# Kernel optimization log

Measured on AMD Instinct MI355X. Metric: run time of the kernel, lower is better.

The kernel has to match this reference:

```python
import jax, jax.numpy as jnp
import numpy as np

VOCAB, EMBED = 50000, 256
MODULES, HEADS, HID = 2, 4, 64
B, S = 8, 2048
LABELS = 16


def setup_inputs() -> dict:
    key = jax.random.key(0)
    ks = jax.random.split(key, 12)
    seqs = jax.random.randint(ks[0], (B, S), 0, VOCAB)
    emb = jax.random.normal(ks[1], (VOCAB, EMBED), jnp.float32) * 0.02
    Wq = jax.random.normal(ks[2], (MODULES, HEADS, HID, EMBED), jnp.float32) * (1.0 / np.sqrt(EMBED))
    bq = jax.random.normal(ks[3], (MODULES, HEADS, HID), jnp.float32) * 0.01
    Wk = jax.random.normal(ks[4], (MODULES, HEADS, HID, EMBED), jnp.float32) * (1.0 / np.sqrt(EMBED))
    bk = jax.random.normal(ks[5], (MODULES, HEADS, HID), jnp.float32) * 0.01
    Wv = jax.random.normal(ks[6], (MODULES, HEADS, HID, EMBED), jnp.float32) * (1.0 / np.sqrt(EMBED))
    bv = jax.random.normal(ks[7], (MODULES, HEADS, HID), jnp.float32) * 0.01
    Wz = jax.random.normal(ks[8], (MODULES, EMBED, HEADS * HID), jnp.float32) * (1.0 / np.sqrt(HEADS * HID))
    bz = jax.random.normal(ks[9], (MODULES, EMBED), jnp.float32) * 0.01
    Wo = jax.random.normal(ks[10], (LABELS, S * EMBED), jnp.float32) * (1.0 / np.sqrt(S * EMBED))
    bo = jax.random.normal(ks[11], (LABELS,), jnp.float32) * 0.01
    return {"seqs": seqs, "emb": emb, "Wq": Wq, "bq": bq, "Wk": Wk, "bk": bk,
            "Wv": Wv, "bv": bv, "Wz": Wz, "bz": bz, "Wo": Wo, "bo": bo}


def _forward(seqs, emb, Wq, bq, Wk, bk, Wv, bv, Wz, bz, Wo, bo):
    x = emb[seqs]  # [B, S, E]
    scale = jnp.float32(EMBED) ** 0.5
    for m in range(MODULES):
        # per-head projections with relu (dropout=0 / eval mode)
        Q = jax.nn.relu(jnp.einsum('bse,hde->bhsd', x, Wq[m]) + bq[m][None, :, None, :])
        K = jax.nn.relu(jnp.einsum('bse,hde->bhsd', x, Wk[m]) + bk[m][None, :, None, :])
        V = jax.nn.relu(jnp.einsum('bse,hde->bhsd', x, Wv[m]) + bv[m][None, :, None, :])
        QK = jnp.einsum('bhsd,bhtd->bhst', Q, K) / scale  # [B,H,S,S]
        # double softmax: first over the query axis (torch dim=1 of [B,S,S]),
        # then over the key axis (torch dim=2)
        A = jax.nn.softmax(QK, axis=2)
        A = jax.nn.softmax(A, axis=3)
        Z = jnp.einsum('bhst,bhtd->bhsd', A, V)  # [B,H,S,HID]
        Zall = jnp.transpose(Z, (0, 2, 1, 3)).reshape(x.shape[0], S, HEADS * HID)
        ZF = jnp.einsum('bsk,ek->bse', Zall, Wz[m]) + bz[m]
        x = ZF + x  # residual (layer_norm=False)
    Xf = x.reshape(x.shape[0], S * EMBED)
    y = jax.nn.sigmoid(Xf @ Wo.T + bo)
    return y


def reference(seqs, emb, Wq, bq, Wk, bk, Wv, bv, Wz, bz, Wo, bo):
    return _forward(seqs, emb, Wq, bq, Wk, bk, Wv, bv, Wz, bz, Wo, bo)
```

## Files before the change

### kernel.cpp

```cpp
#include <hip/hip_runtime.h>
#include <math.h>

#define Bb 8
#define Ss 2048
#define Ee 256
#define Hh 4
#define Dd 64

typedef unsigned short u16;
typedef unsigned int u32;
typedef __attribute__((ext_vector_type(8))) short bf16x8;
typedef __attribute__((ext_vector_type(4))) float f32x4;
typedef __attribute__((ext_vector_type(16))) float f32x16;

__device__ __forceinline__ u16 f2bf(float f) {
  union { float f; u32 u; } c; c.f = f;
  return (u16)((c.u + 0x7FFFu + ((c.u >> 16) & 1u)) >> 16);
}
__device__ __forceinline__ float bf2f(u16 u) {
  union { u32 u; float f; } c; c.u = ((u32)u) << 16;
  return c.f;
}
__device__ __forceinline__ float bf2fs(short s) { return bf2f((u16)s); }
__device__ __forceinline__ u32 cvtpk(float a, float b) {
  u32 r;
  asm("v_cvt_pk_bf16_f32 %0, %1, %2" : "=v"(r) : "v"(a), "v"(b));
  return r;
}
__device__ __forceinline__ float ex2(float x) { return __builtin_amdgcn_exp2f(x); }

__global__ __launch_bounds__(256) void k_w2b(const float* __restrict__ src,
                                             u16* __restrict__ dst) {
  int idx = (blockIdx.x * 256 + threadIdx.x) * 4;
  float4 v = *reinterpret_cast<const float4*>(src + idx);
  ushort4 o;
  o.x = f2bf(v.x); o.y = f2bf(v.y); o.z = f2bf(v.z); o.w = f2bf(v.w);
  *reinterpret_cast<ushort4*>(dst + idx) = o;
}

__global__ __launch_bounds__(256) void k_gather(const int* __restrict__ seqs,
                                                const float* __restrict__ emb,
                                                float* __restrict__ x,
                                                u16* __restrict__ xb) {
  int idx = blockIdx.x * 256 + threadIdx.x;
  int row = idx >> 6, c4 = idx & 63;
  int tok = seqs[row];
  float4 v = reinterpret_cast<const float4*>(emb)[(size_t)tok * 64 + c4];
  reinterpret_cast<float4*>(x)[(size_t)row * 64 + c4] = v;
  ushort4 o;
  o.x = f2bf(v.x); o.y = f2bf(v.y); o.z = f2bf(v.z); o.w = f2bf(v.w);
  reinterpret_cast<ushort4*>(xb)[(size_t)row * 64 + c4] = o;
}

__global__ __launch_bounds__(256) void k_qkvm(const u16* __restrict__ xb,
    const u16* __restrict__ Wqb, const u16* __restrict__ Wkb, const u16* __restrict__ Wvb,
    const float* __restrict__ bq, const float* __restrict__ bk, const float* __restrict__ bv,
    u16* __restrict__ Qf, u16* __restrict__ Kf, u16* __restrict__ Vf, int mod) {
  __shared__ short Xs[128][72];
  __shared__ short Ws[128][72];
  int tid = threadIdx.x;
  int bn = blockIdx.x;
  int arr = bn >> 1, coff = (bn & 1) << 7;
  const u16* W = (arr == 0 ? Wqb : arr == 1 ? Wkb : Wvb) + (size_t)mod * 256 * 256;
  const float* bias = (arr == 0 ? bq : arr == 1 ? bk : bv) + mod * 256;
  u16* Out = (arr == 0 ? Qf : arr == 1 ? Kf : Vf);
  float oscale = (arr == 0) ? 0.0625f * 1.44269504f : 1.0f;
  int s0 = blockIdx.y * 128;
  int lr = tid >> 1, lc = (tid & 1) << 5;
  int w = tid >> 6, lane = tid & 63, ml = lane & 15, q = lane >> 4;
  int sh = (w >> 1) << 6, th = (w & 1) << 6;
  f32x4 acc[4][4] = {};
  for (int k0 = 0; k0 < 256; k0 += 64) {
#pragma unroll
    for (int hh = 0; hh < 4; hh++) {
      *reinterpret_cast<bf16x8*>(&Xs[lr][lc + hh * 8]) =
          *reinterpret_cast<const bf16x8*>(xb + (size_t)(s0 + lr) * Ee + k0 + lc + hh * 8);
      *reinterpret_cast<bf16x8*>(&Ws[lr][lc + hh * 8]) =
          *reinterpret_cast<const bf16x8*>(W + (size_t)(coff + lr) * Ee + k0 + lc + hh * 8);
    }
    __syncthreads();
#pragma unroll
    for (int ks = 0; ks < 2; ks++) {
      bf16x8 af[4], bfr[4];
#pragma unroll
      for (int mt = 0; mt < 4; mt++)
        af[mt] = *reinterpret_cast<const bf16x8*>(&Xs[sh + mt * 16 + ml][ks * 32 + q * 8]);
#pragma unroll
      for (int nt = 0; nt < 4; nt++)
        bfr[nt] = *reinterpret_cast<const bf16x8*>(&Ws[th + nt * 16 + ml][ks * 32 + q * 8]);
#pragma unroll
      for (int mt = 0; mt < 4; mt++)
#pragma unroll
        for (int nt = 0; nt < 4; nt++)
          acc[mt][nt] = __builtin_amdgcn_mfma_f32_16x16x32_bf16(af[mt], bfr[nt], acc[mt][nt], 0, 0, 0);
    }
    __syncthreads();
  }
#pragma unroll
  for (int mt = 0; mt < 4; mt++)
#pragma unroll
    for (int nt = 0; nt < 4; nt++)
#pragma unroll
      for (int r = 0; r < 4; r++) {
        int gm = s0 + sh + mt * 16 + q * 4 + r;
        int cc = coff + th + nt * 16 + ml;
        float v = acc[mt][nt][r] + bias[cc];
        v = (v > 0.f ? v : 0.f) * oscale;
        Out[(size_t)gm * Ee + cc] = f2bf(v);
      }
}

__global__ __launch_bounds__(256) void k_vt(const u16* __restrict__ Vf,
                                            u16* __restrict__ Vt) {
  __shared__ u16 T[64][72];
  int tid = threadIdx.x;
  int t0 = blockIdx.x * 64;
  int z = blockIdx.y;
  int b = z >> 2, h = z & 3;
  int lr = tid >> 2, lc = (tid & 3) << 4;
#pragma unroll
  for (int hh = 0; hh < 2; hh++) {
    bf16x8 v = *reinterpret_cast<const bf16x8*>(
        Vf + (size_t)(b * Ss + t0 + lr) * Ee + h * Dd + lc + hh * 8);
#pragma unroll
    for (int j = 0; j < 8; j++) T[lr][lc + hh * 8 + j] = (u16)v[j];
  }
  __syncthreads();
#pragma unroll
  for (int j = 0; j < 16; j++) {
    Vt[((size_t)z * Dd + lr) * Ss + t0 + lc + j] = T[lc + j][lr];
  }
}

__global__ __launch_bounds__(256) void k_vsum(const u16* __restrict__ Vt,
                                              float* __restrict__ SV,
                                              float* __restrict__ csums) {
  int gi = (blockIdx.y * gridDim.x + blockIdx.x) * 256 + threadIdx.x;
  if (gi < 32 * Ss) csums[gi] = 0.f;
  int z = blockIdx.y;
  int d = blockIdx.x * 4 + (threadIdx.x >> 6);
  int lane = threadIdx.x & 63;
  const u16* row = Vt + ((size_t)z * Dd + d) * Ss;
  float s = 0.f;
#pragma unroll
  for (int it = 0; it < 4; it++) {
    bf16x8 v = *reinterpret_cast<const bf16x8*>(row + it * 512 + lane * 8);
#pragma unroll
    for (int j = 0; j < 8; j++) s += bf2fs(v[j]);
  }
#pragma unroll
  for (int off = 32; off; off >>= 1) s += __shfl_xor(s, off);
  if (lane == 0) SV[(size_t)z * Dd + d] = s;
}

__global__ __launch_bounds__(256, 4) void k_csum(const u16* __restrict__ Qf,
    const u16* __restrict__ Kf, float* __restrict__ csums) {
  __shared__ float csm[2][128];
  int tid = threadIdx.x;
  int lin = (blockIdx.z * 2 + blockIdx.y) * 16 + blockIdx.x;
  int wgid = (lin & 7) * 128 + (lin >> 3);
  int ttile = wgid & 15, shalf = (wgid >> 4) & 1, z = wgid >> 5;
  int b = z >> 2, h = z & 3;
  const u16* Qb = Qf + (size_t)b * Ss * Ee + h * Dd;
  const u16* Kb = Kf + (size_t)b * Ss * Ee + h * Dd;
  int w = tid >> 6, lane = tid & 63, l31 = lane & 31, hi = lane >> 5;
  int sh = (w >> 1) << 6, th = (w & 1) << 6;
  const u16* kr = Kb + (size_t)(ttile * 128 + th + l31) * Ee + hi * 8;
  bf16x8 kb[2][4];
#pragma unroll
  for (int tt = 0; tt < 2; tt++)
#pragma unroll
    for (int kk = 0; kk < 4; kk++)
      kb[tt][kk] = *reinterpret_cast<const bf16x8*>(kr + (size_t)tt * 32 * Ee + kk * 16);
  float cs0 = 0.f, cs1 = 0.f;
  int sBeg = shalf * 1024, sEnd = sBeg + 1024;
  for (int s0 = sBeg; s0 < sEnd; s0 += 128) {
#pragma unroll
    for (int qs = 0; qs < 2; qs++) {
      const u16* Qr = Qb + (size_t)(s0 + sh + qs * 32 + l31) * Ee + hi * 8;
      f32x16 a0 = {}, a1 = {};
      __builtin_amdgcn_s_setprio(1);
#pragma unroll
      for (int kk = 0; kk < 4; kk++) {
        bf16x8 qv = *reinterpret_cast<const bf16x8*>(Qr + kk * 16);
        a0 = __builtin_amdgcn_mfma_f32_32x32x16_bf16(qv, kb[0][kk], a0, 0, 0, 0);
        a1 = __builtin_amdgcn_mfma_f32_32x32x16_bf16(qv, kb[1][kk], a1, 0, 0, 0);
      }
      __builtin_amdgcn_s_setprio(0);
#pragma unroll
      for (int j = 0; j < 16; j++) { cs0 += ex2(a0[j]); cs1 += ex2(a1[j]); }
    }
  }
  cs0 += __shfl_xor(cs0, 32);
  cs1 += __shfl_xor(cs1, 32);
  if (lane < 32) {
    csm[w >> 1][th + l31] = cs0;
    csm[w >> 1][th + 32 + l31] = cs1;
  }
  __syncthreads();
  if (tid < 128)
    atomicAdd(&csums[(size_t)z * Ss + ttile * 128 + tid], csm[0][tid] + csm[1][tid]);
}

__global__ void k_llog(float* __restrict__ llic) {
  int i = blockIdx.x * 256 + threadIdx.x;
  llic[i] = -__log2f(llic[i]);
}

__global__ __launch_bounds__(256, 4) void k_att(const u16* __restrict__ Qf,
    const u16* __restrict__ Kf, const u16* __restrict__ Vt,
    const float* __restrict__ llic, const float* __restrict__ SV,
    u16* __restrict__ Zb) {
  __shared__ short Vs[2][64 * 72];
  __shared__ short A2s[64 * 72];
  __shared__ float rs_s[2][64];
  int tid = threadIdx.x;
  int lin = blockIdx.y * 32 + blockIdx.x;
  int wgid = (lin & 7) * 128 + (lin >> 3);
  int z = wgid >> 5, sblk = wgid & 31;
  int b = z >> 2, h = z & 3;
  const u16* Qb = Qf + (size_t)b * Ss * Ee + h * Dd;
  const u16* Kb = Kf + (size_t)b * Ss * Ee + h * Dd;
  const u16* VtZ = Vt + (size_t)z * Dd * Ss;
  const float* lz = llic + (size_t)z * Ss;
  int s0 = sblk * 64;
  int w = tid >> 6, lane = tid & 63;
  int l31 = lane & 31, hi = lane >> 5;
  int tw = w >> 1, sw = w & 1;
  const u16* qrow = Qb + (size_t)(s0 + sw * 32 + l31) * Ee + hi * 8;
  bf16x8 qb0 = *reinterpret_cast<const bf16x8*>(qrow);
  bf16x8 qb1 = *reinterpret_cast<const bf16x8*>(qrow + 16);
  bf16x8 qb2 = *reinterpret_cast<const bf16x8*>(qrow + 32);
  bf16x8 qb3 = *reinterpret_cast<const bf16x8*>(qrow + 48);
  const u16* krow = Kb + (size_t)(tw * 32 + l31) * Ee + hi * 8;
  bf16x8 kf0 = *reinterpret_cast<const bf16x8*>(krow);
  bf16x8 kf1 = *reinterpret_cast<const bf16x8*>(krow + 16);
  bf16x8 kf2 = *reinterpret_cast<const bf16x8*>(krow + 32);
  bf16x8 kf3 = *reinterpret_cast<const bf16x8*>(krow + 48);
  int sd = tid >> 2, sg = (tid & 3) << 4;
  {
    const u16* vsrc = VtZ + (size_t)sd * Ss + sg;
    *reinterpret_cast<bf16x8*>(&Vs[0][sd * 72 + sg]) = *reinterpret_cast<const bf16x8*>(vsrc);
    *reinterpret_cast<bf16x8*>(&Vs[0][sd * 72 + sg + 8]) = *reinterpret_cast<const bf16x8*>(vsrc + 8);
  }
  f32x16 acc2 = {};
  float rsv = 0.f;
  int pb = 0;
  short* arow = &A2s[(sw * 32 + l31) * 72 + tw * 32];
  const short* a2row = &A2s[(tw * 32 + l31) * 72 + hi * 8];
  for (int t0 = 0; t0 < Ss; t0 += 64) {
    f32x16 at = {};
    __builtin_amdgcn_s_setprio(1);
    at = __builtin_amdgcn_mfma_f32_32x32x16_bf16(kf0, qb0, at, 0, 0, 0);
    at = __builtin_amdgcn_mfma_f32_32x32x16_bf16(kf1, qb1, at, 0, 0, 0);
    at = __builtin_amdgcn_mfma_f32_32x32x16_bf16(kf2, qb2, at, 0, 0, 0);
    at = __builtin_amdgcn_mfma_f32_32x32x16_bf16(kf3, qb3, at, 0, 0, 0);
    __builtin_amdgcn_s_setprio(0);
    int tn = (t0 + 64 < Ss) ? t0 + 64 : 0;
    {
      const u16* krn = krow + (size_t)tn * Ee;
      kf0 = *reinterpret_cast<const bf16x8*>(krn);
      kf1 = *reinterpret_cast<const bf16x8*>(krn + 16);
      kf2 = *reinterpret_cast<const bf16x8*>(krn + 32);
      kf3 = *reinterpret_cast<const bf16x8*>(krn + 48);
    }
#pragma unroll
    for (int g = 0; g < 4; g++) {
      const float4 lc = *reinterpret_cast<const float4*>(lz + t0 + tw * 32 + g * 8 + hi * 4);
      float e0 = ex2(at[g * 4 + 0] + lc.x);
      float e1 = ex2(at[g * 4 + 1] + lc.y);
      float e2 = ex2(at[g * 4 + 2] + lc.z);
      float e3 = ex2(at[g * 4 + 3] + lc.w);
      float p0 = e0 * (1.f + e0 * (0.5f + e0 * (0.166666667f + e0 * 0.0416666667f)));
      float p1 = e1 * (1.f + e1 * (0.5f + e1 * (0.166666667f + e1 * 0.0416666667f)));
      float p2 = e2 * (1.f + e2 * (0.5f + e2 * (0.166666667f + e2 * 0.0416666667f)));
      float p3 = e3 * (1.f + e3 * (0.5f + e3 * (0.166666667f + e3 * 0.0416666667f)));
      rsv += (p0 + p1) + (p2 + p3);
      uint2 pk;
      pk.x = cvtpk(p0, p1);
      pk.y = cvtpk(p2, p3);
      *reinterpret_cast<uint2*>(arow + g * 8 + hi * 4) = pk;
    }
    __syncthreads();
    {
      const u16* vsrc = VtZ + (size_t)sd * Ss + tn + sg;
      bf16x8 v0 = *reinterpret_cast<const bf16x8*>(vsrc);
      bf16x8 v1 = *reinterpret_cast<const bf16x8*>(vsrc + 8);
      short* vdst = &Vs[pb ^ 1][sd * 72 + sg];
      *reinterpret_cast<bf16x8*>(vdst) = v0;
      *reinterpret_cast<bf16x8*>(vdst + 8) = v1;
    }
    {
      const short* vrow = &Vs[pb][(sw * 32 + l31) * 72 + hi * 8];
      __builtin_amdgcn_s_setprio(1);
#pragma unroll
      for (int kk = 0; kk < 4; kk++) {
        bf16x8 af2 = *reinterpret_cast<const bf16x8*>(a2row + kk * 16);
        bf16x8 bvv = *reinterpret_cast<const bf16x8*>(vrow + kk * 16);
        acc2 = __builtin_amdgcn_mfma_f32_32x32x16_bf16(af2, bvv, acc2, 0, 0, 0);
      }
      __builtin_amdgcn_s_setprio(0);
    }
    __syncthreads();
    pb ^= 1;
  }
  rsv += __shfl_xor(rsv, 32);
  if (lane < 32) rs_s[tw][sw * 32 + l31] = rsv;
  __syncthreads();
  float svd = SV[(size_t)z * Dd + sw * 32 + l31];
#pragma unroll
  for (int g = 0; g < 4; g++)
#pragma unroll
    for (int rr = 0; rr < 4; rr++) {
      int row = tw * 32 + g * 8 + hi * 4 + rr;
      float inv = 1.f / (2048.f + rs_s[0][row] + rs_s[1][row]);
      float o = (svd + acc2[g * 4 + rr]) * inv;
      Zb[(size_t)(b * Ss + s0 + row) * Ee + h * Dd + sw * 32 + l31] = f2bf(o);
    }
}

__global__ __launch_bounds__(256) void k_zfm(const u16* __restrict__ Zb,
    const u16* __restrict__ Wzb, const float* __restrict__ bzp,
    float* __restrict__ x, u16* __restrict__ xb, int mod) {
  __shared__ short Zs[128][72];
  __shared__ short Ws[128][72];
  int tid = threadIdx.x;
  int coff = blockIdx.x << 7;
  const u16* W = Wzb + (size_t)mod * 256 * 256;
  const float* bias = bzp + mod * Ee;
  int s0 = blockIdx.y * 128;
  int lr = tid >> 1, lc = (tid & 1) << 5;
  int w = tid >> 6, lane = tid & 63, ml = lane & 15, q = lane >> 4;
  int sh = (w >> 1) << 6, th = (w & 1) << 6;
  f32x4 acc[4][4] = {};
  for (int k0 = 0; k0 < 256; k0 += 64) {
#pragma unroll
    for (int hh = 0; hh < 4; hh++) {
      *reinterpret_cast<bf16x8*>(&Zs[lr][lc + hh * 8]) =
          *reinterpret_cast<const bf16x8*>(Zb + (size_t)(s0 + lr) * Ee + k0 + lc + hh * 8);
      *reinterpret_cast<bf16x8*>(&Ws[lr][lc + hh * 8]) =
          *reinterpret_cast<const bf16x8*>(W + (size_t)(coff + lr) * Ee + k0 + lc + hh * 8);
    }
    __syncthreads();
#pragma unroll
    for (int ks = 0; ks < 2; ks++) {
      bf16x8 af[4], bfr[4];
#pragma unroll
      for (int mt = 0; mt < 4; mt++)
        af[mt] = *reinterpret_cast<const bf16x8*>(&Zs[sh + mt * 16 + ml][ks * 32 + q * 8]);
#pragma unroll
      for (int nt = 0; nt < 4; nt++)
        bfr[nt] = *reinterpret_cast<const bf16x8*>(&Ws[th + nt * 16 + ml][ks * 32 + q * 8]);
#pragma unroll
      for (int mt = 0; mt < 4; mt++)
#pragma unroll
        for (int nt = 0; nt < 4; nt++)
          acc[mt][nt] = __builtin_amdgcn_mfma_f32_16x16x32_bf16(af[mt], bfr[nt], acc[mt][nt], 0, 0, 0);
    }
    __syncthreads();
  }
#pragma unroll
  for (int mt = 0; mt < 4; mt++)
#pragma unroll
    for (int nt = 0; nt < 4; nt++)
#pragma unroll
      for (int r = 0; r < 4; r++) {
        int gm = s0 + sh + mt * 16 + q * 4 + r;
        int gn = coff + th + nt * 16 + ml;
        float xv = x[(size_t)gm * Ee + gn] + acc[mt][nt][r] + bias[gn];
        x[(size_t)gm * Ee + gn] = xv;
        xb[(size_t)gm * Ee + gn] = f2bf(xv);
      }
}

__global__ __launch_bounds__(256) void k_final1(const float* __restrict__ x,
    const float* __restrict__ Wo, float* __restrict__ part) {
  int c = blockIdx.x, l = blockIdx.y, b = blockIdx.z;
  int tid = threadIdx.x;
  const float4* xr = reinterpret_cast<const float4*>(x + (size_t)b * (Ss * Ee) + c * 8192);
  const float4* wr = reinterpret_cast<const float4*>(Wo + (size_t)l * (Ss * Ee) + c * 8192);
  float sum = 0.f;
  for (int i = tid; i < 2048; i += 256) {
    float4 a = xr[i], w = wr[i];
    sum += a.x * w.x + a.y * w.y + a.z * w.z + a.w * w.w;
  }
  __shared__ float red[256];
  red[tid] = sum;
  __syncthreads();
  for (int o = 128; o; o >>= 1) {
    if (tid < o) red[tid] += red[tid + o];
    __syncthreads();
  }
  if (tid == 0) part[((b * 16 + l) << 6) + c] = red[0];
}

__global__ void k_final2(const float* __restrict__ part, const float* __restrict__ bo,
                         float* __restrict__ out) {
  int idx = threadIdx.x;
  int b = idx >> 4, l = idx & 15;
  float s = 0.f;
  for (int c = 0; c < 64; c++) s += part[((b * 16 + l) << 6) + c];
  s += bo[l];
  out[idx] = 1.f / (1.f + __expf(-s));
}

extern "C" void kernel_launch(void* const* d_in, const int* in_sizes, int n_in,
                              void* d_out, int out_size, void* d_ws, size_t ws_size,
                              hipStream_t stream) {
  const int*   seqs = (const int*)d_in[0];
  const float* emb  = (const float*)d_in[1];
  const float* Wq   = (const float*)d_in[2];
  const float* bq   = (const float*)d_in[3];
  const float* Wk   = (const float*)d_in[4];
  const float* bk   = (const float*)d_in[5];
  const float* Wv   = (const float*)d_in[6];
  const float* bv   = (const float*)d_in[7];
  const float* Wz   = (const float*)d_in[8];
  const float* bz   = (const float*)d_in[9];
  const float* Wo   = (const float*)d_in[10];
  const float* bo   = (const float*)d_in[11];
  float* out = (float*)d_out;
  float* ws  = (float*)d_ws;

  float* x    = ws;
  u16*   xb   = (u16*)(ws + 4194304);
  u16*   Qf   = (u16*)(ws + 6291456);
  u16*   Kf   = (u16*)(ws + 8388608);
  u16*   Vf   = (u16*)(ws + 10485760);
  u16*   Vt   = (u16*)(ws + 12582912);
  u16*   Zb   = (u16*)(ws + 14680064);
  float* SV   = ws + 16777216;
  float* part = ws + 16779264;
  u16*   Wqb  = (u16*)(ws + 16787456);
  u16*   Wkb  = (u16*)(ws + 16852992);
  u16*   Wvb  = (u16*)(ws + 16918528);
  u16*   Wzb  = (u16*)(ws + 16984064);
  float* llic = ws + 17049600;

  k_gather<<<(Bb * Ss * 64) / 256, 256, 0, stream>>>(seqs, emb, x, xb);
  k_w2b<<<131072 / 1024, 256, 0, stream>>>(Wq, Wqb);
  k_w2b<<<131072 / 1024, 256, 0, stream>>>(Wk, Wkb);
  k_w2b<<<131072 / 1024, 256, 0, stream>>>(Wv, Wvb);
  k_w2b<<<131072 / 1024, 256, 0, stream>>>(Wz, Wzb);

  for (int m = 0; m < 2; m++) {
    k_qkvm<<<dim3(6, 128), 256, 0, stream>>>(xb, Wqb, Wkb, Wvb, bq, bk, bv, Qf, Kf, Vf, m);
    k_vt<<<dim3(32, 32), 256, 0, stream>>>(Vf, Vt);
    k_vsum<<<dim3(16, 32), 256, 0, stream>>>(Vt, SV, llic);
    k_csum<<<dim3(16, 2, 32), 256, 0, stream>>>(Qf, Kf, llic);
    k_llog<<<256, 256, 0, stream>>>(llic);
    k_att<<<dim3(32, 32), 256, 0, stream>>>(Qf, Kf, Vt, llic, SV, Zb);
    k_zfm<<<dim3(2, 128), 256, 0, stream>>>(Zb, Wzb, bz, x, xb, m);
  }

  k_final1<<<dim3(64, 16, 8), 256, 0, stream>>>(x, Wo, part);
  k_final2<<<1, 128, 0, stream>>>(part, bo, out);
}
```

Baseline: 526.4 us.

## Software-pipeline Q loads in csum, double-buffer attention LDS, restructure final GEMV

```diff
diff --git a/kernel.cpp b/kernel.cpp
--- a/kernel.cpp
+++ b/kernel.cpp
@@ -172,24 +172,33 @@
 #pragma unroll
     for (int kk = 0; kk < 4; kk++)
       kb[tt][kk] = *reinterpret_cast<const bf16x8*>(kr + (size_t)tt * 32 * Ee + kk * 16);
+  const u16* Qr0 = Qb + (size_t)(shalf * 1024 + sh + l31) * Ee + hi * 8;
+  bf16x8 qc0 = *reinterpret_cast<const bf16x8*>(Qr0);
+  bf16x8 qc1 = *reinterpret_cast<const bf16x8*>(Qr0 + 16);
+  bf16x8 qc2 = *reinterpret_cast<const bf16x8*>(Qr0 + 32);
+  bf16x8 qc3 = *reinterpret_cast<const bf16x8*>(Qr0 + 48);
   float cs0 = 0.f, cs1 = 0.f;
-  int sBeg = shalf * 1024, sEnd = sBeg + 1024;
-  for (int s0 = sBeg; s0 < sEnd; s0 += 128) {
-#pragma unroll
-    for (int qs = 0; qs < 2; qs++) {
-      const u16* Qr = Qb + (size_t)(s0 + sh + qs * 32 + l31) * Ee + hi * 8;
-      f32x16 a0 = {}, a1 = {};
-      __builtin_amdgcn_s_setprio(1);
-#pragma unroll
-      for (int kk = 0; kk < 4; kk++) {
-        bf16x8 qv = *reinterpret_cast<const bf16x8*>(Qr + kk * 16);
-        a0 = __builtin_amdgcn_mfma_f32_32x32x16_bf16(qv, kb[0][kk], a0, 0, 0, 0);
-        a1 = __builtin_amdgcn_mfma_f32_32x32x16_bf16(qv, kb[1][kk], a1, 0, 0, 0);
-      }
-      __builtin_amdgcn_s_setprio(0);
-#pragma unroll
-      for (int j = 0; j < 16; j++) { cs0 += ex2(a0[j]); cs1 += ex2(a1[j]); }
-    }
+  for (int it = 0; it < 16; it++) {
+    int itn = (it + 1) & 15;
+    const u16* qnp = Qr0 + (size_t)(((itn >> 1) << 7) + ((itn & 1) << 5)) * Ee;
+    bf16x8 qn0 = *reinterpret_cast<const bf16x8*>(qnp);
+    bf16x8 qn1 = *reinterpret_cast<const bf16x8*>(qnp + 16);
+    bf16x8 qn2 = *reinterpret_cast<const bf16x8*>(qnp + 32);
+    bf16x8 qn3 = *reinterpret_cast<const bf16x8*>(qnp + 48);
+    f32x16 a0 = {}, a1 = {};
+    __builtin_amdgcn_s_setprio(1);
+    a0 = __builtin_amdgcn_mfma_f32_32x32x16_bf16(qc0, kb[0][0], a0, 0, 0, 0);
+    a1 = __builtin_amdgcn_mfma_f32_32x32x16_bf16(qc0, kb[1][0], a1, 0, 0, 0);
+    a0 = __builtin_amdgcn_mfma_f32_32x32x16_bf16(qc1, kb[0][1], a0, 0, 0, 0);
+    a1 = __builtin_amdgcn_mfma_f32_32x32x16_bf16(qc1, kb[1][1], a1, 0, 0, 0);
+    a0 = __builtin_amdgcn_mfma_f32_32x32x16_bf16(qc2, kb[0][2], a0, 0, 0, 0);
+    a1 = __builtin_amdgcn_mfma_f32_32x32x16_bf16(qc2, kb[1][2], a1, 0, 0, 0);
+    a0 = __builtin_amdgcn_mfma_f32_32x32x16_bf16(qc3, kb[0][3], a0, 0, 0, 0);
+    a1 = __builtin_amdgcn_mfma_f32_32x32x16_bf16(qc3, kb[1][3], a1, 0, 0, 0);
+    __builtin_amdgcn_s_setprio(0);
+#pragma unroll
+    for (int j = 0; j < 16; j++) { cs0 += ex2(a0[j]); cs1 += ex2(a1[j]); }
+    qc0 = qn0; qc1 = qn1; qc2 = qn2; qc3 = qn3;
   }
   cs0 += __shfl_xor(cs0, 32);
   cs1 += __shfl_xor(cs1, 32);
@@ -212,7 +221,7 @@
     const float* __restrict__ llic, const float* __restrict__ SV,
     u16* __restrict__ Zb) {
   __shared__ short Vs[2][64 * 72];
-  __shared__ short A2s[64 * 72];
+  __shared__ short A2s[2][64 * 72];
   __shared__ float rs_s[2][64];
   int tid = threadIdx.x;
   int lin = blockIdx.y * 32 + blockIdx.x;
@@ -238,72 +247,75 @@
   bf16x8 kf2 = *reinterpret_cast<const bf16x8*>(krow + 32);
   bf16x8 kf3 = *reinterpret_cast<const bf16x8*>(krow + 48);
   int sd = tid >> 2, sg = (tid & 3) << 4;
-  {
-    const u16* vsrc = VtZ + (size_t)sd * Ss + sg;
-    *reinterpret_cast<bf16x8*>(&Vs[0][sd * 72 + sg]) = *reinterpret_cast<const bf16x8*>(vsrc);
-    *reinterpret_cast<bf16x8*>(&Vs[0][sd * 72 + sg + 8]) = *reinterpret_cast<const bf16x8*>(vsrc + 8);
-  }
+  int vso = sd * 72 + sg;
+  const u16* vbase = VtZ + (size_t)sd * Ss + sg;
+  *reinterpret_cast<bf16x8*>(&Vs[0][vso]) = *reinterpret_cast<const bf16x8*>(vbase);
+  *reinterpret_cast<bf16x8*>(&Vs[0][vso + 8]) = *reinterpret_cast<const bf16x8*>(vbase + 8);
+  bf16x8 vr0 = *reinterpret_cast<const bf16x8*>(vbase + 64);
+  bf16x8 vr1 = *reinterpret_cast<const bf16x8*>(vbase + 64 + 8);
   f32x16 acc2 = {};
   float rsv = 0.f;
-  int pb = 0;
-  short* arow = &A2s[(sw * 32 + l31) * 72 + tw * 32];
-  const short* a2row = &A2s[(tw * 32 + l31) * 72 + hi * 8];
-  for (int t0 = 0; t0 < Ss; t0 += 64) {
-    f32x16 at = {};
-    __builtin_amdgcn_s_setprio(1);
-    at = __builtin_amdgcn_mfma_f32_32x32x16_bf16(kf0, qb0, at, 0, 0, 0);
-    at = __builtin_amdgcn_mfma_f32_32x32x16_bf16(kf1, qb1, at, 0, 0, 0);
-    at = __builtin_amdgcn_mfma_f32_32x32x16_bf16(kf2, qb2, at, 0, 0, 0);
-    at = __builtin_amdgcn_mfma_f32_32x32x16_bf16(kf3, qb3, at, 0, 0, 0);
-    __builtin_amdgcn_s_setprio(0);
-    int tn = (t0 + 64 < Ss) ? t0 + 64 : 0;
-    {
-      const u16* krn = krow + (size_t)tn * Ee;
-      kf0 = *reinterpret_cast<const bf16x8*>(krn);
-      kf1 = *reinterpret_cast<const bf16x8*>(krn + 16);
-      kf2 = *reinterpret_cast<const bf16x8*>(krn + 32);
-      kf3 = *reinterpret_cast<const bf16x8*>(krn + 48);
-    }
-#pragma unroll
-    for (int g = 0; g < 4; g++) {
-      const float4 lc = *reinterpret_cast<const float4*>(lz + t0 + tw * 32 + g * 8 + hi * 4);
-      float e0 = ex2(at[g * 4 + 0] + lc.x);
-      float e1 = ex2(at[g * 4 + 1] + lc.y);
-      float e2 = ex2(at[g * 4 + 2] + lc.z);
-      float e3 = ex2(at[g * 4 + 3] + lc.w);
-      float p0 = e0 * (1.f + e0 * (0.5f + e0 * (0.166666667f + e0 * 0.0416666667f)));
-      float p1 = e1 * (1.f + e1 * (0.5f + e1 * (0.166666667f + e1 * 0.0416666667f)));
-      float p2 = e2 * (1.f + e2 * (0.5f + e2 * (0.166666667f + e2 * 0.0416666667f)));
-      float p3 = e3 * (1.f + e3 * (0.5f + e3 * (0.166666667f + e3 * 0.0416666667f)));
-      rsv += (p0 + p1) + (p2 + p3);
-      uint2 pk;
-      pk.x = cvtpk(p0, p1);
-      pk.y = cvtpk(p2, p3);
-      *reinterpret_cast<uint2*>(arow + g * 8 + hi * 4) = pk;
-    }
-    __syncthreads();
-    {
-      const u16* vsrc = VtZ + (size_t)sd * Ss + tn + sg;
-      bf16x8 v0 = *reinterpret_cast<const bf16x8*>(vsrc);
-      bf16x8 v1 = *reinterpret_cast<const bf16x8*>(vsrc + 8);
-      short* vdst = &Vs[pb ^ 1][sd * 72 + sg];
-      *reinterpret_cast<bf16x8*>(vdst) = v0;
-      *reinterpret_cast<bf16x8*>(vdst + 8) = v1;
-    }
-    {
-      const short* vrow = &Vs[pb][(sw * 32 + l31) * 72 + hi * 8];
-      __builtin_amdgcn_s_setprio(1);
-#pragma unroll
-      for (int kk = 0; kk < 4; kk++) {
-        bf16x8 af2 = *reinterpret_cast<const bf16x8*>(a2row + kk * 16);
-        bf16x8 bvv = *reinterpret_cast<const bf16x8*>(vrow + kk * 16);
-        acc2 = __builtin_amdgcn_mfma_f32_32x32x16_bf16(af2, bvv, acc2, 0, 0, 0);
-      }
-      __builtin_amdgcn_s_setprio(0);
-    }
-    __syncthreads();
-    pb ^= 1;
-  }
+  const int arowo = (sw * 32 + l31) * 72 + tw * 32;
+  const int a2rowo = (tw * 32 + l31) * 72 + hi * 8;
+  const int vrowo = (sw * 32 + l31) * 72 + hi * 8;
+  __syncthreads();
+
+#define CHUNK(T0, PB) { \
+    const float* lcp = lz + (T0) + tw * 32 + hi * 4; \
+    float4 lcv0 = *reinterpret_cast<const float4*>(lcp); \
+    float4 lcv1 = *reinterpret_cast<const float4*>(lcp + 8); \
+    float4 lcv2 = *reinterpret_cast<const float4*>(lcp + 16); \
+    float4 lcv3 = *reinterpret_cast<const float4*>(lcp + 24); \
+    f32x16 at = {}; \
+    __builtin_amdgcn_s_setprio(1); \
+    at = __builtin_amdgcn_mfma_f32_32x32x16_bf16(kf0, qb0, at, 0, 0, 0); \
+    at = __builtin_amdgcn_mfma_f32_32x32x16_bf16(kf1, qb1, at, 0, 0, 0); \
+    at = __builtin_amdgcn_mfma_f32_32x32x16_bf16(kf2, qb2, at, 0, 0, 0); \
+    at = __builtin_amdgcn_mfma_f32_32x32x16_bf16(kf3, qb3, at, 0, 0, 0); \
+    __builtin_amdgcn_s_setprio(0); \
+    int tn = ((T0) + 64) & (Ss - 1); \
+    { const u16* krn = krow + (size_t)tn * Ee; \
+      kf0 = *reinterpret_cast<const bf16x8*>(krn); \
+      kf1 = *reinterpret_cast<const bf16x8*>(krn + 16); \
+      kf2 = *reinterpret_cast<const bf16x8*>(krn + 32); \
+      kf3 = *reinterpret_cast<const bf16x8*>(krn + 48); } \
+    float4 lcv[4] = {lcv0, lcv1, lcv2, lcv3}; \
+    _Pragma("unroll") \
+    for (int g = 0; g < 4; g++) { \
+      float e0 = ex2(at[g * 4 + 0] + lcv[g].x); \
+      float e1 = ex2(at[g * 4 + 1] + lcv[g].y); \
+      float e2 = ex2(at[g * 4 + 2] + lcv[g].z); \
+      float e3 = ex2(at[g * 4 + 3] + lcv[g].w); \
+      float p0 = e0 * (1.f + e0 * (0.5f + e0 * (0.166666667f + e0 * 0.0416666667f))); \
+      float p1 = e1 * (1.f + e1 * (0.5f + e1 * (0.166666667f + e1 * 0.0416666667f))); \
+      float p2 = e2 * (1.f + e2 * (0.5f + e2 * (0.166666667f + e2 * 0.0416666667f))); \
+      float p3 = e3 * (1.f + e3 * (0.5f + e3 * (0.166666667f + e3 * 0.0416666667f))); \
+      rsv += (p0 + p1) + (p2 + p3); \
+      uint2 pk; pk.x = cvtpk(p0, p1); pk.y = cvtpk(p2, p3); \
+      *reinterpret_cast<uint2*>(&A2s[PB][arowo + g * 8 + hi * 4]) = pk; \
+    } \
+    __syncthreads(); \
+    *reinterpret_cast<bf16x8*>(&Vs[(PB) ^ 1][vso]) = vr0; \
+    *reinterpret_cast<bf16x8*>(&Vs[(PB) ^ 1][vso + 8]) = vr1; \
+    __builtin_amdgcn_s_setprio(1); \
+    _Pragma("unroll") \
+    for (int kk = 0; kk < 4; kk++) { \
+      bf16x8 af2 = *reinterpret_cast<const bf16x8*>(&A2s[PB][a2rowo + kk * 16]); \
+      bf16x8 bvv = *reinterpret_cast<const bf16x8*>(&Vs[PB][vrowo + kk * 16]); \
+      acc2 = __builtin_amdgcn_mfma_f32_32x32x16_bf16(af2, bvv, acc2, 0, 0, 0); \
+    } \
+    __builtin_amdgcn_s_setprio(0); \
+    { int tv = ((T0) + 128) & (Ss - 1); \
+      vr0 = *reinterpret_cast<const bf16x8*>(vbase + tv); \
+      vr1 = *reinterpret_cast<const bf16x8*>(vbase + tv + 8); } \
+  }
+
+  for (int t0 = 0; t0 < Ss; t0 += 128) {
+    CHUNK(t0, 0);
+    CHUNK(t0 + 64, 1);
+  }
+#undef CHUNK
+
   rsv += __shfl_xor(rsv, 32);
   if (lane < 32) rs_s[tw][sw * 32 + l31] = rsv;
   __syncthreads();
@@ -375,32 +387,53 @@
 
 __global__ __launch_bounds__(256) void k_final1(const float* __restrict__ x,
     const float* __restrict__ Wo, float* __restrict__ part) {
-  int c = blockIdx.x, l = blockIdx.y, b = blockIdx.z;
-  int tid = threadIdx.x;
-  const float4* xr = reinterpret_cast<const float4*>(x + (size_t)b * (Ss * Ee) + c * 8192);
-  const float4* wr = reinterpret_cast<const float4*>(Wo + (size_t)l * (Ss * Ee) + c * 8192);
-  float sum = 0.f;
-  for (int i = tid; i < 2048; i += 256) {
-    float4 a = xr[i], w = wr[i];
-    sum += a.x * w.x + a.y * w.y + a.z * w.z + a.w * w.w;
-  }
-  __shared__ float red[256];
-  red[tid] = sum;
+  int cb = blockIdx.x;
+  int b0 = blockIdx.y * 2;
+  int tid = threadIdx.x;
+  int w = tid >> 6, lane = tid & 63;
+  float acc[2][16];
+#pragma unroll
+  for (int bb = 0; bb < 2; bb++)
+#pragma unroll
+    for (int l = 0; l < 16; l++) acc[bb][l] = 0.f;
+  const float4* x4 = reinterpret_cast<const float4*>(x);
+  const float4* w4 = reinterpret_cast<const float4*>(Wo);
+#pragma unroll
+  for (int it = 0; it < 4; it++) {
+    int i = it * 256 + tid;
+    float4 xv0 = x4[(size_t)(b0 + 0) * 131072 + cb * 1024 + i];
+    float4 xv1 = x4[(size_t)(b0 + 1) * 131072 + cb * 1024 + i];
+#pragma unroll
+    for (int l = 0; l < 16; l++) {
+      float4 wv = w4[(size_t)l * 131072 + cb * 1024 + i];
+      acc[0][l] += xv0.x * wv.x + xv0.y * wv.y + xv0.z * wv.z + xv0.w * wv.w;
+      acc[1][l] += xv1.x * wv.x + xv1.y * wv.y + xv1.z * wv.z + xv1.w * wv.w;
+    }
+  }
+  __shared__ float red[4][32];
+#pragma unroll
+  for (int bb = 0; bb < 2; bb++)
+#pragma unroll
+    for (int l = 0; l < 16; l++) {
+      float v = acc[bb][l];
+#pragma unroll
+      for (int off = 1; off < 64; off <<= 1) v += __shfl_xor(v, off);
+      if (lane == 0) red[w][bb * 16 + l] = v;
+    }
   __syncthreads();
-  for (int o = 128; o; o >>= 1) {
-    if (tid < o) red[tid] += red[tid + o];
-    __syncthreads();
-  }
-  if (tid == 0) part[((b * 16 + l) << 6) + c] = red[0];
+  if (tid < 32) {
+    int lb = tid >> 4, l = tid & 15;
+    float s = red[0][tid] + red[1][tid] + red[2][tid] + red[3][tid];
+    part[(size_t)((b0 + lb) * 16 + l) * 128 + cb] = s;
+  }
 }
 
 __global__ void k_final2(const float* __restrict__ part, const float* __restrict__ bo,
                          float* __restrict__ out) {
   int idx = threadIdx.x;
-  int b = idx >> 4, l = idx & 15;
   float s = 0.f;
-  for (int c = 0; c < 64; c++) s += part[((b * 16 + l) << 6) + c];
-  s += bo[l];
+  for (int c = 0; c < 128; c++) s += part[(size_t)idx * 128 + c];
+  s += bo[idx & 15];
   out[idx] = 1.f / (1.f + __expf(-s));
 }
 
@@ -430,12 +463,12 @@
   u16*   Vt   = (u16*)(ws + 12582912);
   u16*   Zb   = (u16*)(ws + 14680064);
   float* SV   = ws + 16777216;
-  float* part = ws + 16779264;
   u16*   Wqb  = (u16*)(ws + 16787456);
   u16*   Wkb  = (u16*)(ws + 16852992);
   u16*   Wvb  = (u16*)(ws + 16918528);
   u16*   Wzb  = (u16*)(ws + 16984064);
   float* llic = ws + 17049600;
+  float* part = ws + 6291456;
 
   k_gather<<<(Bb * Ss * 64) / 256, 256, 0, stream>>>(seqs, emb, x, xb);
   k_w2b<<<131072 / 1024, 256, 0, stream>>>(Wq, Wqb);
@@ -453,6 +486,6 @@
     k_zfm<<<dim3(2, 128), 256, 0, stream>>>(Zb, Wzb, bz, x, xb, m);
   }
 
-  k_final1<<<dim3(64, 16, 8), 256, 0, stream>>>(x, Wo, part);
+  k_final1<<<dim3(128, 4), 256, 0, stream>>>(x, Wo, part);
   k_final2<<<1, 128, 0, stream>>>(part, bo, out);
 }
```

Result: slower. 677.0 us (+28.6%).
